# Kernel tuning notes

Hardware: AMD Instinct MI355X
Metric: run time of the kernel (lower is better)

The kernel has to match this reference:

```python
import jax, jax.numpy as jnp
import numpy as np

L, B, D = 2048, 2, 1024
H, DK, DV = 16, 64, 64
SPAN = 128
LN_EPS = 1e-5


def setup_inputs() -> dict:
    key = jax.random.key(0)
    ks = jax.random.split(key, 8)
    s_qk = np.sqrt(2.0 / (D + DK)).astype(np.float32)
    s_v = np.sqrt(2.0 / (D + DV)).astype(np.float32)
    return {
        "query": jax.random.normal(ks[0], (L, B, D), jnp.float32),
        "key": jax.random.normal(ks[1], (L, B, D), jnp.float32),
        "value": jax.random.normal(ks[2], (L, B, D), jnp.float32),
        "Wq": jax.random.normal(ks[3], (D, H * DK), jnp.float32) * s_qk,
        "bq": jnp.zeros((H * DK,), jnp.float32),
        "Wk": jax.random.normal(ks[4], (D, H * DK), jnp.float32) * s_qk,
        "bk": jnp.zeros((H * DK,), jnp.float32),
        "Wv": jax.random.normal(ks[5], (D, H * DV), jnp.float32) * s_v,
        "bv": jnp.zeros((H * DV,), jnp.float32),
        "Wfc": jax.random.normal(ks[6], (H * DV, D), jnp.float32) * np.sqrt(2.0 / (H * DV + D)).astype(np.float32),
        "bfc": jnp.zeros((D,), jnp.float32),
        "gamma": jnp.ones((D,), jnp.float32),
        "beta": jnp.zeros((D,), jnp.float32),
    }


def reference(query, key, value, Wq, bq, Wk, bk, Wv, bv, Wfc, bfc, gamma, beta):
    l, b, d = query.shape
    # projections: (l,b,H*dk) -> (H,b,l,dk)   [torch rearrange 'l b (head k) -> head b l k']
    q = (query @ Wq + bq).reshape(l, b, H, DK).transpose(2, 1, 0, 3)
    k = (key @ Wk + bk).reshape(l, b, H, DK).transpose(2, 1, 0, 3)
    v = (value @ Wv + bv).reshape(l, b, H, DV).transpose(2, 1, 0, 3)
    scores = jnp.einsum("hblk,hbtk->hblt", q, k) / jnp.sqrt(jnp.float32(DK))
    # banded additive mask: keep |j - i| <= SPAN
    idx = jnp.arange(l)
    band = jnp.abs(idx[None, :] - idx[:, None]) <= SPAN  # (l, l)
    scores = jnp.where(band[None, None], scores, -jnp.inf)
    attn = jax.nn.softmax(scores, axis=-1)
    out = jnp.einsum("hblt,hbtv->hblv", attn, v)
    # 'head b l v -> l b (head v)'
    out = out.transpose(2, 1, 0, 3).reshape(l, b, H * DV)
    out = out @ Wfc + bfc  # dropout p=0.0 -> identity
    y = out + query  # residual
    mu = jnp.mean(y, axis=-1, keepdims=True)
    var = jnp.mean(jnp.square(y - mu), axis=-1, keepdims=True)
    y = (y - mu) * jax.lax.rsqrt(var + LN_EPS) * gamma + beta
    return (y, attn)
```

## Files before the change

kernel.cpp:

```cpp
#include <hip/hip_runtime.h>
#include <stdint.h>

#define L_SEQ 2048
#define BB 2
#define DD 1024
#define NH 16
#define SPAN 128

typedef __attribute__((ext_vector_type(8))) short short8;
typedef __attribute__((ext_vector_type(4))) float floatx4;

__device__ __forceinline__ short f32_bf16(float f) {
  uint32_t u = __float_as_uint(f);
  u += 0x7FFFu + ((u >> 16) & 1u);
  return (short)(u >> 16);
}
__device__ __forceinline__ float bf2f(short s) {
  return __uint_as_float(((uint32_t)(uint16_t)s) << 16);
}

__device__ __forceinline__ void gld16(const short* g, short* l) {
  __builtin_amdgcn_global_load_lds(
      (__attribute__((address_space(1))) void*)(g),
      (__attribute__((address_space(3))) void*)(l), 16, 0, 0);
}

__global__ __launch_bounds__(256) void k_prep(
    const float* __restrict__ s0, const float* __restrict__ s1, const float* __restrict__ s2,
    const float* __restrict__ w0, const float* __restrict__ w1,
    const float* __restrict__ w2, const float* __restrict__ w3,
    short* __restrict__ d0, short* __restrict__ d1, short* __restrict__ d2,
    short* __restrict__ WT) {
  __shared__ float tile[64][65];
  int bid = blockIdx.x, tid = threadIdx.x;
  if (bid < 12288) {
    int y = bid >> 12;
    const float* s = y == 0 ? s0 : (y == 1 ? s1 : s2);
    short* d = y == 0 ? d0 : (y == 1 ? d1 : d2);
    int i = (bid & 4095) * 256 + tid;
    float4 v = ((const float4*)s)[i];
    short4 o;
    o.x = f32_bf16(v.x); o.y = f32_bf16(v.y); o.z = f32_bf16(v.z); o.w = f32_bf16(v.w);
    ((short4*)d)[i] = o;
  } else {
    int b2 = bid - 12288;
    int z = b2 >> 8;
    int xy = b2 & 255;
    int bx = (xy & 15) * 64, by = (xy >> 4) * 64;
    int tx = tid & 63, ty = tid >> 6;
    const float* src = z == 0 ? w0 : z == 1 ? w1 : z == 2 ? w2 : w3;
    short* out = WT + (size_t)z * (DD * DD);
#pragma unroll
    for (int r = 0; r < 64; r += 4)
      tile[ty + r][tx] = src[(size_t)(by + ty + r) * DD + bx + tx];
    __syncthreads();
    int r2 = tid >> 2, q = tid & 3;
    short8 o0, o1;
#pragma unroll
    for (int j = 0; j < 8; ++j) o0[j] = f32_bf16(tile[q * 16 + j][r2]);
#pragma unroll
    for (int j = 0; j < 8; ++j) o1[j] = f32_bf16(tile[q * 16 + 8 + j][r2]);
    *(short8*)(out + (size_t)(bx + r2) * DD + by + q * 16) = o0;
    *(short8*)(out + (size_t)(bx + r2) * DD + by + q * 16 + 8) = o1;
  }
}

#define BM 128
#define BN 128
#define SMEM_SH 17408

__device__ __forceinline__ void gemm_core(const short* __restrict__ A,
                                          const short* __restrict__ BT,
                                          floatx4 acc[4][4], int bm0, int bn0,
                                          short* smem) {
  int tid = threadIdx.x;
  int wave = tid >> 6, lane = tid & 63;
  int li = lane & 15, quad = lane >> 4;
  int wm = (wave & 1) * 64, wn = (wave >> 1) * 64;
  int r0 = wave * 32 + (lane >> 2);
  int c0 = (lane & 3) * 8;
  const short* gA = A + (size_t)(bm0 + r0) * DD + c0;
  const short* gB = BT + (size_t)(bn0 + r0) * DD + c0;
  short* sA = smem;
  short* sB = smem + 8192;
  {
    short* lA = sA + wave * 1024;
    short* lB = sB + wave * 1024;
    gld16(gA, lA);
    gld16(gA + (size_t)16 * DD, lA + 512);
    gld16(gB, lB);
    gld16(gB + (size_t)16 * DD, lB + 512);
  }
  __syncthreads();
#pragma unroll 2
  for (int k = 0; k < 32; ++k) {
    int cur = k & 1;
    if (k < 31) {
      int koff = (k + 1) * 32;
      short* lA = sA + (cur ^ 1) * 4096 + wave * 1024;
      short* lB = sB + (cur ^ 1) * 4096 + wave * 1024;
      gld16(gA + koff, lA);
      gld16(gA + (size_t)16 * DD + koff, lA + 512);
      gld16(gB + koff, lB);
      gld16(gB + (size_t)16 * DD + koff, lB + 512);
    }
    const short* cA = sA + cur * 4096;
    const short* cB = sB + cur * 4096;
    short8 af[4], bf[4];
#pragma unroll
    for (int t = 0; t < 4; ++t) {
      af[t] = *(const short8*)&cA[(wm + t * 16 + li) * 32 + quad * 8];
      bf[t] = *(const short8*)&cB[(wn + t * 16 + li) * 32 + quad * 8];
    }
#pragma unroll
    for (int tm = 0; tm < 4; ++tm)
#pragma unroll
      for (int tn = 0; tn < 4; ++tn)
        acc[tm][tn] = __builtin_amdgcn_mfma_f32_16x16x32_bf16(af[tm], bf[tn], acc[tm][tn], 0, 0, 0);
    __syncthreads();
  }
}

__global__ __launch_bounds__(256) void k_proj(
    const short* __restrict__ xq, const short* __restrict__ xk, const short* __restrict__ xv,
    const short* __restrict__ WT,
    const float* __restrict__ bq, const float* __restrict__ bk, const float* __restrict__ bv,
    short* __restrict__ qo, short* __restrict__ ko, short* __restrict__ vto) {
  __shared__ __attribute__((aligned(16))) short smem[SMEM_SH];
  int flat = (blockIdx.z * 32 + blockIdx.y) * 8 + blockIdx.x;
  int swz = (flat & 7) * 96 + (flat >> 3);
  int bxw = swz & 7, byw = (swz >> 3) & 31, mode = swz >> 8;
  const short* A = mode == 0 ? xq : (mode == 1 ? xk : xv);
  const short* BT = WT + (size_t)mode * DD * DD;
  const float* bias = mode == 0 ? bq : (mode == 1 ? bk : bv);
  floatx4 acc[4][4] = {};
  int bm0 = byw * BM, bn0 = bxw * BN;
  gemm_core(A, BT, acc, bm0, bn0, smem);

  int tid = threadIdx.x;
  int wave = tid >> 6, lane = tid & 63;
  int li = lane & 15, quad = lane >> 4;
  int wm = (wave & 1) * 64, wn = (wave >> 1) * 64;
#pragma unroll
  for (int tm = 0; tm < 4; ++tm)
#pragma unroll
    for (int tn = 0; tn < 4; ++tn) {
      int gn = bn0 + wn + tn * 16 + li;
      float bs = bias[gn];
#pragma unroll
      for (int r = 0; r < 4; ++r)
        smem[(wm + tm * 16 + quad * 4 + r) * 136 + wn + tn * 16 + li] =
            f32_bf16(acc[tm][tn][r] + bs);
    }
  __syncthreads();
  if (mode != 2) {
    short* dst = (mode == 0) ? qo : ko;
    int row = tid >> 1, half = tid & 1;
    int gm = bm0 + row, l = gm >> 1, b = gm & 1;
    int h = (bn0 + half * 64) >> 6;
    short* drow = dst + (((size_t)h * BB + b) * L_SEQ + l) * 64;
#pragma unroll
    for (int j = 0; j < 8; ++j)
      *(short8*)(drow + j * 8) = *(const short8*)&smem[row * 136 + half * 64 + j * 8];
  } else {
    int col = tid & 127, b2 = tid >> 7;
    int h2 = (bn0 + col) >> 6, dv = (bn0 + col) & 63;
    int l0 = bm0 >> 1;
    short* drow = vto + (((size_t)h2 * BB + b2) * 64 + dv) * L_SEQ + l0;
#pragma unroll
    for (int u0 = 0; u0 < 64; u0 += 8) {
      short8 o;
#pragma unroll
      for (int j = 0; j < 8; ++j)
        o[j] = smem[(2 * (u0 + j) + b2) * 136 + col];
      *(short8*)(drow + u0) = o;
    }
  }
}

__global__ __launch_bounds__(256) void k_attn(
    const short* __restrict__ qw, const short* __restrict__ kw, const short* __restrict__ vTw,
    float* __restrict__ attn_out, short* __restrict__ ctx) {
  __shared__ short sbuf[20480];
  short* K0 = sbuf;
  short* K1 = sbuf + 10240;
  const int tid = threadIdx.x;
  const int wv = tid >> 6, lane = tid & 63;
  const int li = lane & 15, quad = lane >> 4;
  int flat = blockIdx.y * 32 + blockIdx.x;
  int swz = (flat & 7) * 128 + (flat >> 3);
  const int i0b = (swz & 31) * 64;
  const int hb = swz >> 5;
  const int i0 = i0b + wv * 16;
  const int jb = i0b - SPAN;
  const short* Q = qw + (size_t)hb * L_SEQ * 64;
  const short* K = kw + (size_t)hb * L_SEQ * 64;
  const short* VT = vTw + (size_t)hb * 64 * L_SEQ;
  float* Aout = attn_out + (size_t)hb * L_SEQ * L_SEQ;

#pragma unroll
  for (int t = 0; t < 10; ++t) {
    int idx = wv + 4 * t;
    int half = idx >= 20 ? 1 : 0;
    int ridx = idx - half * 20;
    int row = ridx * 16 + (lane >> 2);
    int jr = jb + row;
    int jc = jr < 0 ? 0 : (jr >= L_SEQ ? L_SEQ - 1 : jr);
    const short* g = K + (size_t)jc * 64 + half * 32 + (lane & 3) * 8;
    short* l = (half ? K1 : K0) + ridx * 16 * 32;
    gld16(g, l);
  }

  short8 qf0 = *(const short8*)(Q + (size_t)(i0 + li) * 64 + quad * 8);
  short8 qf1 = *(const short8*)(Q + (size_t)(i0 + li) * 64 + 32 + quad * 8);
  __syncthreads();

  floatx4 S[17];
  const int jbase = i0 - SPAN;
  __builtin_amdgcn_s_setprio(1);
#pragma unroll
  for (int t = 0; t < 17; ++t) {
    int j0 = jbase + t * 16;
    floatx4 acc = {0.f, 0.f, 0.f, 0.f};
    if (j0 > -16 && j0 < L_SEQ) {
      int jrel = (wv + t) * 16;
      short8 kf0 = *(const short8*)&K0[(jrel + li) * 32 + quad * 8];
      short8 kf1 = *(const short8*)&K1[(jrel + li) * 32 + quad * 8];
      acc = __builtin_amdgcn_mfma_f32_16x16x32_bf16(qf0, kf0, acc, 0, 0, 0);
      acc = __builtin_amdgcn_mfma_f32_16x16x32_bf16(qf1, kf1, acc, 0, 0, 0);
    }
    S[t] = acc;
  }
  __builtin_amdgcn_s_setprio(0);
  float mrow[4] = {-1e30f, -1e30f, -1e30f, -1e30f};
#pragma unroll
  for (int t = 0; t < 17; ++t) {
    int j = jbase + t * 16 + li;
#pragma unroll
    for (int r = 0; r < 4; ++r) {
      int i = i0 + quad * 4 + r;
      bool inband = (j >= i - SPAN) && (j <= i + SPAN) && (j >= 0) && (j < L_SEQ);
      float s = inband ? S[t][r] * 0.125f : -1e30f;
      S[t][r] = s;
      mrow[r] = fmaxf(mrow[r], s);
    }
  }
#pragma unroll
  for (int m = 1; m <= 8; m <<= 1)
#pragma unroll
    for (int r = 0; r < 4; ++r) mrow[r] = fmaxf(mrow[r], __shfl_xor(mrow[r], m));
  float lsum[4] = {0.f, 0.f, 0.f, 0.f};
#pragma unroll
  for (int t = 0; t < 17; ++t)
#pragma unroll
    for (int r = 0; r < 4; ++r) {
      float p = __expf(S[t][r] - mrow[r]);
      S[t][r] = p;
      lsum[r] += p;
    }
#pragma unroll
  for (int m = 1; m <= 8; m <<= 1)
#pragma unroll
    for (int r = 0; r < 4; ++r) lsum[r] += __shfl_xor(lsum[r], m);
  float inv[4];
#pragma unroll
  for (int r = 0; r < 4; ++r) inv[r] = 1.0f / lsum[r];

  __syncthreads();
  short* myP = sbuf + wv * 4736;
#pragma unroll
  for (int t = 0; t < 17; ++t)
#pragma unroll
    for (int r = 0; r < 4; ++r)
      myP[(quad * 4 + r) * 296 + t * 16 + li] = f32_bf16(S[t][r] * inv[r]);
  *(short4*)&myP[(lane >> 2) * 296 + 272 + (lane & 3) * 4] = short4{0, 0, 0, 0};
  __syncthreads();

  floatx4 O[4] = {};
#pragma unroll
  for (int c = 0; c < 9; ++c) {
    short8 pf = *(const short8*)&myP[li * 296 + c * 32 + quad * 8];
    int jg = jbase + c * 32 + quad * 8;
    int jc = (jg >= 0 && jg < L_SEQ) ? jg : 0;
    short8 vf[4];
#pragma unroll
    for (int n = 0; n < 4; ++n)
      vf[n] = *(const short8*)(VT + (size_t)(n * 16 + li) * L_SEQ + jc);
    __builtin_amdgcn_s_setprio(1);
#pragma unroll
    for (int n = 0; n < 4; ++n)
      O[n] = __builtin_amdgcn_mfma_f32_16x16x32_bf16(pf, vf[n], O[n], 0, 0, 0);
    __builtin_amdgcn_s_setprio(0);
  }
  const int b = hb & 1, h = hb >> 1;
#pragma unroll
  for (int n = 0; n < 4; ++n)
#pragma unroll
    for (int r = 0; r < 4; ++r) {
      int irow = quad * 4 + r;
      ctx[((size_t)(i0 + irow) * BB + b) * DD + h * 64 + n * 16 + li] = f32_bf16(O[n][r]);
    }

#pragma unroll 4
  for (int row = 0; row < 16; ++row) {
    float* orow = Aout + (size_t)(i0 + row) * L_SEQ;
    const short* prow = &myP[row * 296];
#pragma unroll
    for (int it = 0; it < 8; ++it) {
      int col = it * 256 + lane * 4;
      int s = col - jbase;
      floatx4 v = {0.f, 0.f, 0.f, 0.f};
      if (s >= 0 && s < 288) {
        short4 p4 = *(const short4*)(prow + s);
        v.x = bf2f(p4.x); v.y = bf2f(p4.y); v.z = bf2f(p4.z); v.w = bf2f(p4.w);
      }
      __builtin_nontemporal_store(v, (floatx4*)(orow + col));
    }
  }
}

__global__ __launch_bounds__(256) void k_fc(
    const short* __restrict__ ctx, const short* __restrict__ WfcT,
    const float* __restrict__ bfc, const float* __restrict__ query,
    float* __restrict__ ypre) {
  __shared__ __attribute__((aligned(16))) short smem[SMEM_SH];
  int flat = blockIdx.y * 8 + blockIdx.x;
  int swz = (flat & 7) * 32 + (flat >> 3);
  int bm0 = (swz >> 3) * BM, bn0 = (swz & 7) * BN;
  floatx4 acc[4][4] = {};
  gemm_core(ctx, WfcT, acc, bm0, bn0, smem);
  int tid = threadIdx.x;
  int wave = tid >> 6, lane = tid & 63;
  int li = lane & 15, quad = lane >> 4;
  int wn = (wave >> 1) * 64;
  float* ft = (float*)smem;
#pragma unroll
  for (int hrow = 0; hrow < 2; ++hrow) {
    __syncthreads();
    if ((wave & 1) == hrow) {
#pragma unroll
      for (int tm = 0; tm < 4; ++tm)
#pragma unroll
        for (int tn = 0; tn < 4; ++tn) {
          int gn = bn0 + wn + tn * 16 + li;
          float bs = bfc[gn];
#pragma unroll
          for (int r = 0; r < 4; ++r)
            ft[(tm * 16 + quad * 4 + r) * 136 + wn + tn * 16 + li] = acc[tm][tn][r] + bs;
        }
    }
    __syncthreads();
    int row = tid >> 2, c0 = (tid & 3) * 32;
    int gm = bm0 + hrow * 64 + row;
    const float4* q4 = (const float4*)(query + (size_t)gm * DD + bn0 + c0);
    float4* o4 = (float4*)(ypre + (size_t)gm * DD + bn0 + c0);
#pragma unroll
    for (int v = 0; v < 8; ++v) {
      float4 a = *(const float4*)&ft[row * 136 + c0 + v * 4];
      float4 qq = q4[v];
      float4 o;
      o.x = a.x + qq.x; o.y = a.y + qq.y; o.z = a.z + qq.z; o.w = a.w + qq.w;
      o4[v] = o;
    }
  }
}

__global__ __launch_bounds__(256) void k_ln(
    const float* __restrict__ yp, const float* __restrict__ gamma,
    const float* __restrict__ beta, float* __restrict__ out) {
  __shared__ float red[8];
  int row = blockIdx.x, tid = threadIdx.x;
  float4 v = ((const float4*)(yp + (size_t)row * DD))[tid];
  float s = v.x + v.y + v.z + v.w;
  float s2 = v.x * v.x + v.y * v.y + v.z * v.z + v.w * v.w;
#pragma unroll
  for (int m = 1; m <= 32; m <<= 1) {
    s += __shfl_xor(s, m);
    s2 += __shfl_xor(s2, m);
  }
  int wv = tid >> 6;
  if ((tid & 63) == 0) { red[wv] = s; red[wv + 4] = s2; }
  __syncthreads();
  s = red[0] + red[1] + red[2] + red[3];
  s2 = red[4] + red[5] + red[6] + red[7];
  float mu = s * (1.0f / DD);
  float var = s2 * (1.0f / DD) - mu * mu;
  float rs = rsqrtf(var + 1e-5f);
  float4 g = ((const float4*)gamma)[tid];
  float4 bb = ((const float4*)beta)[tid];
  float4 o;
  o.x = (v.x - mu) * rs * g.x + bb.x;
  o.y = (v.y - mu) * rs * g.y + bb.y;
  o.z = (v.z - mu) * rs * g.z + bb.z;
  o.w = (v.w - mu) * rs * g.w + bb.w;
  ((float4*)(out + (size_t)row * DD))[tid] = o;
}

extern "C" void kernel_launch(void* const* d_in, const int* in_sizes, int n_in,
                              void* d_out, int out_size, void* d_ws, size_t ws_size,
                              hipStream_t stream) {
  const float* query = (const float*)d_in[0];
  const float* key   = (const float*)d_in[1];
  const float* value = (const float*)d_in[2];
  const float* Wq    = (const float*)d_in[3];
  const float* bq    = (const float*)d_in[4];
  const float* Wk    = (const float*)d_in[5];
  const float* bk    = (const float*)d_in[6];
  const float* Wv    = (const float*)d_in[7];
  const float* bv    = (const float*)d_in[8];
  const float* Wfc   = (const float*)d_in[9];
  const float* bfc   = (const float*)d_in[10];
  const float* gamma = (const float*)d_in[11];
  const float* beta  = (const float*)d_in[12];
  float* out = (float*)d_out;
  float* attn = out + (size_t)L_SEQ * BB * DD;

  char* w = (char*)d_ws;
  short* xq_b  = (short*)(w);
  short* xk_b  = (short*)(w + ((size_t)8 << 20));
  short* xv_b  = (short*)(w + ((size_t)16 << 20));
  short* WT    = (short*)(w + ((size_t)24 << 20));
  short* q_ws  = (short*)(w + ((size_t)32 << 20));
  short* k_ws  = (short*)(w + ((size_t)40 << 20));
  short* vT_ws = (short*)(w + ((size_t)56 << 20));
  short* ctx   = (short*)(w + ((size_t)64 << 20));
  float* ypre  = (float*)(w + ((size_t)72 << 20));

  k_prep<<<13312, 256, 0, stream>>>(query, key, value, Wq, Wk, Wv, Wfc,
                                    xq_b, xk_b, xv_b, WT);
  k_proj<<<dim3(8, 32, 3), 256, 0, stream>>>(xq_b, xk_b, xv_b, WT, bq, bk, bv, q_ws, k_ws, vT_ws);
  k_attn<<<dim3(32, 32), 256, 0, stream>>>(q_ws, k_ws, vT_ws, attn, ctx);
  k_attn<<<dim3(32, 32), 256, 0, stream>>>(q_ws, k_ws, vT_ws, attn, ctx);
  k_fc<<<dim3(8, 32), 256, 0, stream>>>(ctx, WT + (size_t)3 * DD * DD, bfc, query, ypre);
  k_ln<<<4096, 256, 0, stream>>>(ypre, gamma, beta, out);
}
```

Measured before the change: 822.0 us.

## Fuse activation bf16 conversion into projection GEMM and drop duplicate attention launch

The projection GEMM now reads the fp32 query/key/value directly and converts them to bf16 in registers before storing into LDS, with register prefetch of the next k-slice. This removes the separate cast pass and its bf16 round-trip through memory; the prep kernel now only transposes the weights. A redundant second launch of the attention kernel is also removed. The register-staged A path adds VALU and register pressure inside the GEMM loop and loses the async global-to-LDS load for A.

After: 732.4 us. -10.9%, faster.

```diff
diff --git a/kernel.cpp b/kernel.cpp
--- a/kernel.cpp
+++ b/kernel.cpp
@@ -18,6 +18,12 @@
 __device__ __forceinline__ float bf2f(short s) {
   return __uint_as_float(((uint32_t)(uint16_t)s) << 16);
 }
+__device__ __forceinline__ short8 pack8(float4 x, float4 y) {
+  short8 r;
+  r[0] = f32_bf16(x.x); r[1] = f32_bf16(x.y); r[2] = f32_bf16(x.z); r[3] = f32_bf16(x.w);
+  r[4] = f32_bf16(y.x); r[5] = f32_bf16(y.y); r[6] = f32_bf16(y.z); r[7] = f32_bf16(y.w);
+  return r;
+}
 
 __device__ __forceinline__ void gld16(const short* g, short* l) {
   __builtin_amdgcn_global_load_lds(
@@ -26,43 +32,29 @@
 }
 
 __global__ __launch_bounds__(256) void k_prep(
-    const float* __restrict__ s0, const float* __restrict__ s1, const float* __restrict__ s2,
     const float* __restrict__ w0, const float* __restrict__ w1,
     const float* __restrict__ w2, const float* __restrict__ w3,
-    short* __restrict__ d0, short* __restrict__ d1, short* __restrict__ d2,
     short* __restrict__ WT) {
   __shared__ float tile[64][65];
   int bid = blockIdx.x, tid = threadIdx.x;
-  if (bid < 12288) {
-    int y = bid >> 12;
-    const float* s = y == 0 ? s0 : (y == 1 ? s1 : s2);
-    short* d = y == 0 ? d0 : (y == 1 ? d1 : d2);
-    int i = (bid & 4095) * 256 + tid;
-    float4 v = ((const float4*)s)[i];
-    short4 o;
-    o.x = f32_bf16(v.x); o.y = f32_bf16(v.y); o.z = f32_bf16(v.z); o.w = f32_bf16(v.w);
-    ((short4*)d)[i] = o;
-  } else {
-    int b2 = bid - 12288;
-    int z = b2 >> 8;
-    int xy = b2 & 255;
-    int bx = (xy & 15) * 64, by = (xy >> 4) * 64;
-    int tx = tid & 63, ty = tid >> 6;
-    const float* src = z == 0 ? w0 : z == 1 ? w1 : z == 2 ? w2 : w3;
-    short* out = WT + (size_t)z * (DD * DD);
-#pragma unroll
-    for (int r = 0; r < 64; r += 4)
-      tile[ty + r][tx] = src[(size_t)(by + ty + r) * DD + bx + tx];
-    __syncthreads();
-    int r2 = tid >> 2, q = tid & 3;
-    short8 o0, o1;
-#pragma unroll
-    for (int j = 0; j < 8; ++j) o0[j] = f32_bf16(tile[q * 16 + j][r2]);
-#pragma unroll
-    for (int j = 0; j < 8; ++j) o1[j] = f32_bf16(tile[q * 16 + 8 + j][r2]);
-    *(short8*)(out + (size_t)(bx + r2) * DD + by + q * 16) = o0;
-    *(short8*)(out + (size_t)(bx + r2) * DD + by + q * 16 + 8) = o1;
-  }
+  int z = bid >> 8;
+  int xy = bid & 255;
+  int bx = (xy & 15) * 64, by = (xy >> 4) * 64;
+  int tx = tid & 63, ty = tid >> 6;
+  const float* src = z == 0 ? w0 : z == 1 ? w1 : z == 2 ? w2 : w3;
+  short* out = WT + (size_t)z * (DD * DD);
+#pragma unroll
+  for (int r = 0; r < 64; r += 4)
+    tile[ty + r][tx] = src[(size_t)(by + ty + r) * DD + bx + tx];
+  __syncthreads();
+  int r2 = tid >> 2, q = tid & 3;
+  short8 o0, o1;
+#pragma unroll
+  for (int j = 0; j < 8; ++j) o0[j] = f32_bf16(tile[q * 16 + j][r2]);
+#pragma unroll
+  for (int j = 0; j < 8; ++j) o1[j] = f32_bf16(tile[q * 16 + 8 + j][r2]);
+  *(short8*)(out + (size_t)(bx + r2) * DD + by + q * 16) = o0;
+  *(short8*)(out + (size_t)(bx + r2) * DD + by + q * 16 + 8) = o1;
 }
 
 #define BM 128
@@ -121,8 +113,71 @@
   }
 }
 
+__device__ __forceinline__ void gemm_core_f32a(const float* __restrict__ A,
+                                               const short* __restrict__ BT,
+                                               floatx4 acc[4][4], int bm0, int bn0,
+                                               short* smem) {
+  int tid = threadIdx.x;
+  int wave = tid >> 6, lane = tid & 63;
+  int li = lane & 15, quad = lane >> 4;
+  int wm = (wave & 1) * 64, wn = (wave >> 1) * 64;
+  int r0 = wave * 32 + (lane >> 2);
+  int c0 = (lane & 3) * 8;
+  const float* gA = A + (size_t)(bm0 + r0) * DD + c0;
+  const short* gB = BT + (size_t)(bn0 + r0) * DD + c0;
+  short* sA = smem;
+  short* sB = smem + 8192;
+  short* wAbase = sA + wave * 1024 + lane * 8;
+  {
+    float4 a0 = *(const float4*)(gA);
+    float4 a1 = *(const float4*)(gA + 4);
+    float4 a2 = *(const float4*)(gA + (size_t)16 * DD);
+    float4 a3 = *(const float4*)(gA + (size_t)16 * DD + 4);
+    *(short8*)(wAbase) = pack8(a0, a1);
+    *(short8*)(wAbase + 512) = pack8(a2, a3);
+    short* lB = sB + wave * 1024;
+    gld16(gB, lB);
+    gld16(gB + (size_t)16 * DD, lB + 512);
+  }
+  __syncthreads();
+#pragma unroll 2
+  for (int k = 0; k < 32; ++k) {
+    int cur = k & 1;
+    float4 a0, a1, a2, a3;
+    if (k < 31) {
+      int koff = (k + 1) * 32;
+      a0 = *(const float4*)(gA + koff);
+      a1 = *(const float4*)(gA + koff + 4);
+      a2 = *(const float4*)(gA + (size_t)16 * DD + koff);
+      a3 = *(const float4*)(gA + (size_t)16 * DD + koff + 4);
+      short* lB = sB + (cur ^ 1) * 4096 + wave * 1024;
+      gld16(gB + koff, lB);
+      gld16(gB + (size_t)16 * DD + koff, lB + 512);
+    }
+    const short* cA = sA + cur * 4096;
+    const short* cB = sB + cur * 4096;
+    short8 af[4], bf[4];
+#pragma unroll
+    for (int t = 0; t < 4; ++t) {
+      af[t] = *(const short8*)&cA[(wm + t * 16 + li) * 32 + quad * 8];
+      bf[t] = *(const short8*)&cB[(wn + t * 16 + li) * 32 + quad * 8];
+    }
+#pragma unroll
+    for (int tm = 0; tm < 4; ++tm)
+#pragma unroll
+      for (int tn = 0; tn < 4; ++tn)
+        acc[tm][tn] = __builtin_amdgcn_mfma_f32_16x16x32_bf16(af[tm], bf[tn], acc[tm][tn], 0, 0, 0);
+    if (k < 31) {
+      short* wA = sA + (cur ^ 1) * 4096 + wave * 1024 + lane * 8;
+      *(short8*)(wA) = pack8(a0, a1);
+      *(short8*)(wA + 512) = pack8(a2, a3);
+    }
+    __syncthreads();
+  }
+}
+
 __global__ __launch_bounds__(256) void k_proj(
-    const short* __restrict__ xq, const short* __restrict__ xk, const short* __restrict__ xv,
+    const float* __restrict__ xq, const float* __restrict__ xk, const float* __restrict__ xv,
     const short* __restrict__ WT,
     const float* __restrict__ bq, const float* __restrict__ bk, const float* __restrict__ bv,
     short* __restrict__ qo, short* __restrict__ ko, short* __restrict__ vto) {
@@ -130,12 +185,12 @@
   int flat = (blockIdx.z * 32 + blockIdx.y) * 8 + blockIdx.x;
   int swz = (flat & 7) * 96 + (flat >> 3);
   int bxw = swz & 7, byw = (swz >> 3) & 31, mode = swz >> 8;
-  const short* A = mode == 0 ? xq : (mode == 1 ? xk : xv);
+  const float* A = mode == 0 ? xq : (mode == 1 ? xk : xv);
   const short* BT = WT + (size_t)mode * DD * DD;
   const float* bias = mode == 0 ? bq : (mode == 1 ? bk : bv);
   floatx4 acc[4][4] = {};
   int bm0 = byw * BM, bn0 = bxw * BN;
-  gemm_core(A, BT, acc, bm0, bn0, smem);
+  gemm_core_f32a(A, BT, acc, bm0, bn0, smem);
 
   int tid = threadIdx.x;
   int wave = tid >> 6, lane = tid & 63;
@@ -416,9 +471,6 @@
   float* attn = out + (size_t)L_SEQ * BB * DD;
 
   char* w = (char*)d_ws;
-  short* xq_b  = (short*)(w);
-  short* xk_b  = (short*)(w + ((size_t)8 << 20));
-  short* xv_b  = (short*)(w + ((size_t)16 << 20));
   short* WT    = (short*)(w + ((size_t)24 << 20));
   short* q_ws  = (short*)(w + ((size_t)32 << 20));
   short* k_ws  = (short*)(w + ((size_t)40 << 20));
@@ -426,10 +478,8 @@
   short* ctx   = (short*)(w + ((size_t)64 << 20));
   float* ypre  = (float*)(w + ((size_t)72 << 20));
 
-  k_prep<<<13312, 256, 0, stream>>>(query, key, value, Wq, Wk, Wv, Wfc,
-                                    xq_b, xk_b, xv_b, WT);
-  k_proj<<<dim3(8, 32, 3), 256, 0, stream>>>(xq_b, xk_b, xv_b, WT, bq, bk, bv, q_ws, k_ws, vT_ws);
-  k_attn<<<dim3(32, 32), 256, 0, stream>>>(q_ws, k_ws, vT_ws, attn, ctx);
+  k_prep<<<1024, 256, 0, stream>>>(Wq, Wk, Wv, Wfc, WT);
+  k_proj<<<dim3(8, 32, 3), 256, 0, stream>>>(query, key, value, WT, bq, bk, bv, q_ws, k_ws, vT_ws);
   k_attn<<<dim3(32, 32), 256, 0, stream>>>(q_ws, k_ws, vT_ws, attn, ctx);
   k_fc<<<dim3(8, 32), 256, 0, stream>>>(ctx, WT + (size_t)3 * DD * DD, bfc, query, ypre);
   k_ln<<<4096, 256, 0, stream>>>(ypre, gamma, beta, out);
```
